# Kernel tuning notes

Measured on AMD Instinct MI355X. Metric: run time of the kernel, lower is better.

The kernel has to match this reference:

```python
import jax, jax.numpy as jnp
import numpy as np

NEG_SLOPE = 0.2  # LeakyReLU slope used by GAT attention
EPS = 1e-16


def segment_softmax(scores, seg, num_segments):
    # numerically-stable softmax over edges grouped by destination node
    m = jax.ops.segment_max(scores, seg, num_segments=num_segments)
    ex = jnp.exp(scores - m[seg])
    s = jax.ops.segment_sum(ex, seg, num_segments=num_segments)
    return ex / (s[seg] + EPS)


def gat_conv(x, edge_index, W, a_src, a_dst, b):
    # x: [N, d_in], edge_index: [2, E], W: [d_in, d_out], a_*: [d_out], b: [d_out]
    n = x.shape[0]
    h = x @ W                                   # [N, d_out]
    src, dst = edge_index[0], edge_index[1]     # [E], [E]
    alpha_src = h @ a_src                       # [N]
    alpha_dst = h @ a_dst                       # [N]
    e = jax.nn.leaky_relu(alpha_src[src] + alpha_dst[dst], NEG_SLOPE)  # [E]
    alpha = segment_softmax(e, dst, n)          # [E]
    out = jax.ops.segment_sum(h[src] * alpha[:, None], dst, num_segments=n)  # [N, d_out]
    return out + b


def setup_inputs() -> dict:
    key = jax.random.key(0)
    ks = jax.random.split(key, 12)
    N, D, E = 100000, 64, 1600000
    x = jax.random.normal(ks[0], (N, D), dtype=jnp.float32)
    edge_index = jax.random.randint(ks[1], (2, E), 0, N, dtype=jnp.int64)
    s = 1.0 / np.sqrt(D)
    W1 = jax.random.normal(ks[2], (D, D), dtype=jnp.float32) * s
    a_src1 = jax.random.normal(ks[3], (D,), dtype=jnp.float32) * s
    a_dst1 = jax.random.normal(ks[4], (D,), dtype=jnp.float32) * s
    b1 = jnp.zeros((D,), dtype=jnp.float32)
    W2 = jax.random.normal(ks[5], (D, D), dtype=jnp.float32) * s
    a_src2 = jax.random.normal(ks[6], (D,), dtype=jnp.float32) * s
    a_dst2 = jax.random.normal(ks[7], (D,), dtype=jnp.float32) * s
    b2 = jnp.zeros((D,), dtype=jnp.float32)
    return {"x": x, "edge_index": edge_index,
            "W1": W1, "a_src1": a_src1, "a_dst1": a_dst1, "b1": b1,
            "W2": W2, "a_src2": a_src2, "a_dst2": a_dst2, "b2": b2}


def reference(x, edge_index, W1, a_src1, a_dst1, b1, W2, a_src2, a_dst2, b2):
    # Encoder.forward: conv_near on first 500 edges, conv_include on the rest
    x = gat_conv(x, edge_index[:, :500], W1, a_src1, a_dst1, b1)
    return gat_conv(x, edge_index[:, 500:], W2, a_src2, a_dst2, b2)
```

## Files before the change

kernel.cpp:

```cpp
#include <hip/hip_runtime.h>


#define LRELU(v) ((v) >= 0.0f ? (v) : 0.2f * (v))
#define EPSF 1e-16f
#define NB 128
#define BCAP 512
#define HSZ 1024

struct P {
    const float* x; const int* EI; int E, N;
    const float *W1, *a_src1, *a_dst1, *b1, *W2, *a_src2, *a_dst2, *b2;
    float* F;
    int* bcnt;
    int* map2;
    float* s_spec;
    float* adsp;
    char* stat;
    int* pkey;
    float* as2tab; float* ad2tab; float* h2tab;
    int* slw; int* nxt;
    float4* out;
    int initBlocks;
};

__device__ __forceinline__ float wred_sum(float v) {
    for (int o = 32; o; o >>= 1) v += __shfl_xor(v, o);
    return v;
}
__device__ __forceinline__ int wred_min(int v) {
    for (int o = 32; o; o >>= 1) v = min(v, __shfl_xor(v, o));
    return v;
}

__global__ __launch_bounds__(256) void k1(P p) {
    const int tid = blockIdx.x * 256 + threadIdx.x;
    const int nth = p.initBlocks * 256;
    for (int i = tid; i < p.N; i += nth) { p.map2[i] = -1; p.s_spec[i] = 0.f; p.stat[i] = 0; }
    for (int i = tid; i < NB * 16; i += nth) p.bcnt[i] = 0;

    const int w = tid >> 6, lane = threadIdx.x & 63;
    if (w >= 500) return;

    float wsl = 0.f, wdl = 0.f, hbl = 0.f;
    for (int l = 0; l < 64; ++l) {
        wsl += p.W1[lane * 64 + l] * p.a_src1[l];
        wdl += p.W1[lane * 64 + l] * p.a_dst1[l];
    }
    for (int k = 0; k < 64; ++k) hbl += p.b1[k] * p.W2[k * 64 + lane];

    if (w == 0) {
        p.F[128 + lane] = hbl;
        float asb = wred_sum(hbl * p.a_src2[lane]);
        float adb = wred_sum(hbl * p.a_dst2[lane]);
        if (lane == 0) { p.F[192] = asb; p.F[193] = adb; }
    }

    const int d = p.EI[p.E + w];
    int firstj = 1 << 30;
    for (int r = 0; r < 8; ++r) {
        int j = r * 64 + lane;
        if (j < 500 && p.EI[p.E + j] == d) firstj = min(firstj, j);
    }
    firstj = wred_min(firstj);
    const bool owner = (firstj == w);
    if (lane == 0) p.pkey[w] = owner ? d : -1;
    if (!owner) return;

    const float dv = wred_sum(p.x[(long)d * 64 + lane] * wdl);
    float Ssum = 0.f, e1w = 0.f, x1l = 0.f;
    bool fm = true;
    for (int r = 0; r < 8; ++r) {
        int j = r * 64 + lane;
        bool m = (j < 500) && (p.EI[p.E + j] == d);
        unsigned long long mask = __ballot(m);
        while (mask) {
            int j0 = r * 64 + (int)__ffsll(mask) - 1;
            mask &= mask - 1;
            int sj = p.EI[j0];
            float xs = p.x[(long)sj * 64 + lane];
            float e1j = LRELU(wred_sum(xs * wsl) + dv);
            float ew;
            if (fm) { e1w = e1j; ew = 1.f; fm = false; }
            else ew = expf(e1j - e1w);
            Ssum += ew;
            float h1l = 0.f;
            #pragma unroll
            for (int k = 0; k < 64; ++k) h1l = fmaf(__shfl(xs, k), p.W1[k * 64 + lane], h1l);
            x1l = fmaf(ew, h1l, x1l);
        }
    }
    float x1 = x1l / (Ssum + EPSF) + p.b1[lane];
    float h2l = 0.f;
    #pragma unroll
    for (int k = 0; k < 64; ++k) h2l = fmaf(__shfl(x1, k), p.W2[k * 64 + lane], h2l);
    p.h2tab[w * 64 + lane] = h2l - hbl;
    float as = wred_sum(h2l * p.a_src2[lane]);
    float ad = wred_sum(h2l * p.a_dst2[lane]);
    if (lane == 0) { p.as2tab[w] = as; p.ad2tab[w] = ad; }
}

__device__ __forceinline__ int hlookup(const int* hkey, const int* hval, int x) {
    unsigned idx = ((unsigned)x * 2654435761u) >> 22;
    while (true) {
        int k = hkey[idx];
        if (k == -1) return -1;
        if (k == x) return hval[idx];
        idx = (idx + 1) & (HSZ - 1);
    }
}

__device__ __forceinline__ void specEdge(const P& p, long e, int s, int bkt,
                                         float asb, float adb,
                                         const int* hkey, const int* hval) {
    int sl = hlookup(hkey, hval, s);
    if (sl < 0) return;
    int d = p.EI[p.E + e];
    int jd = hlookup(hkey, hval, d);
    float ad2v = (jd >= 0) ? p.ad2tab[jd] : adb;
    float md  = LRELU(asb + ad2v);
    float esp = LRELU(p.as2tab[sl] + ad2v);
    atomicAdd(&p.s_spec[d], expf(esp - md) - 1.0f);
    p.stat[d] = 2;
    p.adsp[d] = ad2v;
    int i = atomicAdd(&p.bcnt[bkt * 16], 1);
    if (i < BCAP) {
        int pos = bkt * BCAP + i;
        p.slw[pos] = sl;
        p.nxt[pos] = atomicExch(&p.map2[d], pos);
    }
}

__global__ __launch_bounds__(256) void k2(P p) {
    __shared__ int hkey[HSZ];
    __shared__ int hval[HSZ];
    for (int i = threadIdx.x; i < HSZ; i += 256) hkey[i] = -1;
    __syncthreads();
    for (int i = threadIdx.x; i < 500; i += 256) {
        int key = p.pkey[i];
        if (key >= 0) {
            unsigned idx = ((unsigned)key * 2654435761u) >> 22;
            while (true) {
                int old = atomicCAS(&hkey[idx], -1, key);
                if (old == -1) { hval[idx] = i; break; }
                idx = (idx + 1) & (HSZ - 1);
            }
        }
    }
    __syncthreads();
    const float asb = p.F[192], adb = p.F[193];
    long q = (long)blockIdx.x * 256 + threadIdx.x;
    long base = 500 + q * 4;
    if (base >= p.E) return;
    int bkt = (int)(q & (NB - 1));
    if (base + 3 < p.E) {
        int4 s4 = *(const int4*)(p.EI + base);
        specEdge(p, base + 0, s4.x, bkt, asb, adb, hkey, hval);
        specEdge(p, base + 1, s4.y, bkt, asb, adb, hkey, hval);
        specEdge(p, base + 2, s4.z, bkt, asb, adb, hkey, hval);
        specEdge(p, base + 3, s4.w, bkt, asb, adb, hkey, hval);
    } else {
        for (long e = base; e < p.E; ++e) specEdge(p, e, p.EI[e], bkt, asb, adb, hkey, hval);
    }
}

__device__ __forceinline__ void dstEdge(const P& p, int d) {
    char st = p.stat[d];
    if (st == 0) p.stat[d] = 1;
    else if (st == 2) atomicAdd(&p.s_spec[d], 1.0f);
}

__global__ __launch_bounds__(256) void k3(P p) {
    long q = (long)blockIdx.x * 256 + threadIdx.x;
    long base = 500 + q * 4;
    if (base >= p.E) return;
    if (base + 3 < p.E) {
        int4 d4 = *(const int4*)(p.EI + p.E + base);
        dstEdge(p, d4.x); dstEdge(p, d4.y); dstEdge(p, d4.z); dstEdge(p, d4.w);
    } else {
        for (long e = base; e < p.E; ++e) dstEdge(p, p.EI[p.E + e]);
    }
}

__global__ __launch_bounds__(256) void k4(P p) {
    long t = (long)blockIdx.x * 256 + threadIdx.x;
    if (t >= (long)p.N * 16) return;
    int n = (int)(t >> 4), qq = (int)(t & 15);
    char st = p.stat[n];
    float coef = (st != 0) ? 1.0f : 0.0f;
    float4 hb4 = ((const float4*)(p.F + 128))[qq];
    float4 b24 = ((const float4*)p.b2)[qq];
    float4 o;
    o.x = b24.x + coef * hb4.x; o.y = b24.y + coef * hb4.y;
    o.z = b24.z + coef * hb4.z; o.w = b24.w + coef * hb4.w;
    if (st == 2) {
        float den = p.s_spec[n] + EPSF;
        float ad2v = p.adsp[n];
        float md = LRELU(p.F[192] + ad2v);
        int pos = p.map2[n];
        while (pos >= 0) {
            int sl = p.slw[pos];
            float w = expf(LRELU(p.as2tab[sl] + ad2v) - md) / den;
            float4 h4 = ((const float4*)(p.h2tab + sl * 64))[qq];
            o.x = fmaf(w, h4.x, o.x); o.y = fmaf(w, h4.y, o.y);
            o.z = fmaf(w, h4.z, o.z); o.w = fmaf(w, h4.w, o.w);
            pos = p.nxt[pos];
        }
    }
    p.out[t] = o;
}

extern "C" void kernel_launch(void* const* d_in, const int* in_sizes, int n_in,
                              void* d_out, int out_size, void* d_ws, size_t ws_size,
                              hipStream_t stream) {
    P p;
    p.x      = (const float*)d_in[0];
    p.EI     = (const int*)d_in[1];
    p.W1     = (const float*)d_in[2];
    p.a_src1 = (const float*)d_in[3];
    p.a_dst1 = (const float*)d_in[4];
    p.b1     = (const float*)d_in[5];
    p.W2     = (const float*)d_in[6];
    p.a_src2 = (const float*)d_in[7];
    p.a_dst2 = (const float*)d_in[8];
    p.b2     = (const float*)d_in[9];
    p.out    = (float4*)d_out;
    p.N = in_sizes[0] / 64;
    p.E = in_sizes[1] / 2;

    char* base = (char*)d_ws;
    p.F      = (float*)base;
    p.bcnt   = (int*)(base + 1024);
    p.map2   = p.bcnt + NB * 16;
    p.s_spec = (float*)(p.map2 + p.N);
    p.adsp   = p.s_spec + p.N;
    p.stat   = (char*)(p.adsp + p.N);
    char* q  = p.stat + p.N;
    q = (char*)(((uintptr_t)q + 63) & ~(uintptr_t)63);
    p.pkey   = (int*)q;
    p.as2tab = (float*)(p.pkey + 512);
    p.ad2tab = p.as2tab + 512;
    p.h2tab  = p.ad2tab + 512;
    p.slw    = (int*)(p.h2tab + 512 * 64);
    p.nxt    = p.slw + NB * BCAP;

    p.initBlocks = (p.N + 255) / 256;

    long quads = ((long)p.E - 500 + 3) / 4;
    int scanBlocks = (int)((quads + 255) / 256);

    k1<<<p.initBlocks, 256, 0, stream>>>(p);
    k2<<<scanBlocks, 256, 0, stream>>>(p);
    k3<<<scanBlocks, 256, 0, stream>>>(p);
    k4<<<(int)(((long)p.N * 16 + 255) / 256), 256, 0, stream>>>(p);
}
```

Baseline: 65.13 us.

## Replace per-block shared hash table with dense global node-index map

Each of the ~6000 scan blocks used to rebuild a 1024-entry shared-memory hash table from the 500 layer-1 keys and probe it for every edge. The change writes a dense N-sized idx_map in global memory from the layer-1 kernel, so each edge does a direct indexed load instead of a hash probe. To make that map valid before the scan, the fused init/layer-1 kernel is split into a separate init kernel and a layer-1 kernel, which adds one launch. The idx_map lookups are random global reads (400KB, likely cache-resident) in place of LDS probes.

```diff
diff --git a/kernel.cpp b/kernel.cpp
--- a/kernel.cpp
+++ b/kernel.cpp
@@ -5,22 +5,20 @@
 #define EPSF 1e-16f
 #define NB 128
 #define BCAP 512
-#define HSZ 1024
 
 struct P {
     const float* x; const int* EI; int E, N;
     const float *W1, *a_src1, *a_dst1, *b1, *W2, *a_src2, *a_dst2, *b2;
     float* F;
     int* bcnt;
+    int* idx_map;
     int* map2;
     float* s_spec;
     float* adsp;
     char* stat;
-    int* pkey;
     float* as2tab; float* ad2tab; float* h2tab;
     int* slw; int* nxt;
     float4* out;
-    int initBlocks;
 };
 
 __device__ __forceinline__ float wred_sum(float v) {
@@ -32,13 +30,24 @@
     return v;
 }
 
-__global__ __launch_bounds__(256) void k1(P p) {
-    const int tid = blockIdx.x * 256 + threadIdx.x;
-    const int nth = p.initBlocks * 256;
-    for (int i = tid; i < p.N; i += nth) { p.map2[i] = -1; p.s_spec[i] = 0.f; p.stat[i] = 0; }
-    for (int i = tid; i < NB * 16; i += nth) p.bcnt[i] = 0;
-
-    const int w = tid >> 6, lane = threadIdx.x & 63;
+__global__ __launch_bounds__(256) void initk(P p) {
+    int i = blockIdx.x * 256 + threadIdx.x;
+    if (i < p.N) { p.idx_map[i] = -1; p.map2[i] = -1; p.s_spec[i] = 0.f; p.stat[i] = 0; }
+    if (i < NB * 16) p.bcnt[i] = 0;
+    if (blockIdx.x == 0 && threadIdx.x < 64) {
+        int t = threadIdx.x;
+        float hb = 0.f;
+        for (int k = 0; k < 64; ++k) hb += p.b1[k] * p.W2[k * 64 + t];
+        p.F[128 + t] = hb;
+        float as = wred_sum(hb * p.a_src2[t]);
+        float ad = wred_sum(hb * p.a_dst2[t]);
+        if (t == 0) { p.F[192] = as; p.F[193] = ad; }
+    }
+}
+
+__global__ __launch_bounds__(256) void l1k(P p) {
+    const int w = (blockIdx.x * 256 + threadIdx.x) >> 6;
+    const int lane = threadIdx.x & 63;
     if (w >= 500) return;
 
     float wsl = 0.f, wdl = 0.f, hbl = 0.f;
@@ -47,13 +56,6 @@
         wdl += p.W1[lane * 64 + l] * p.a_dst1[l];
     }
     for (int k = 0; k < 64; ++k) hbl += p.b1[k] * p.W2[k * 64 + lane];
-
-    if (w == 0) {
-        p.F[128 + lane] = hbl;
-        float asb = wred_sum(hbl * p.a_src2[lane]);
-        float adb = wred_sum(hbl * p.a_dst2[lane]);
-        if (lane == 0) { p.F[192] = asb; p.F[193] = adb; }
-    }
 
     const int d = p.EI[p.E + w];
     int firstj = 1 << 30;
@@ -62,9 +64,8 @@
         if (j < 500 && p.EI[p.E + j] == d) firstj = min(firstj, j);
     }
     firstj = wred_min(firstj);
-    const bool owner = (firstj == w);
-    if (lane == 0) p.pkey[w] = owner ? d : -1;
-    if (!owner) return;
+    if (firstj != w) return;
+    if (lane == 0) p.idx_map[d] = w;
 
     const float dv = wred_sum(p.x[(long)d * 64 + lane] * wdl);
     float Ssum = 0.f, e1w = 0.f, x1l = 0.f;
@@ -99,23 +100,12 @@
     if (lane == 0) { p.as2tab[w] = as; p.ad2tab[w] = ad; }
 }
 
-__device__ __forceinline__ int hlookup(const int* hkey, const int* hval, int x) {
-    unsigned idx = ((unsigned)x * 2654435761u) >> 22;
-    while (true) {
-        int k = hkey[idx];
-        if (k == -1) return -1;
-        if (k == x) return hval[idx];
-        idx = (idx + 1) & (HSZ - 1);
-    }
-}
-
 __device__ __forceinline__ void specEdge(const P& p, long e, int s, int bkt,
-                                         float asb, float adb,
-                                         const int* hkey, const int* hval) {
-    int sl = hlookup(hkey, hval, s);
+                                         float asb, float adb) {
+    int sl = p.idx_map[s];
     if (sl < 0) return;
     int d = p.EI[p.E + e];
-    int jd = hlookup(hkey, hval, d);
+    int jd = p.idx_map[d];
     float ad2v = (jd >= 0) ? p.ad2tab[jd] : adb;
     float md  = LRELU(asb + ad2v);
     float esp = LRELU(p.as2tab[sl] + ad2v);
@@ -130,36 +120,20 @@
     }
 }
 
-__global__ __launch_bounds__(256) void k2(P p) {
-    __shared__ int hkey[HSZ];
-    __shared__ int hval[HSZ];
-    for (int i = threadIdx.x; i < HSZ; i += 256) hkey[i] = -1;
-    __syncthreads();
-    for (int i = threadIdx.x; i < 500; i += 256) {
-        int key = p.pkey[i];
-        if (key >= 0) {
-            unsigned idx = ((unsigned)key * 2654435761u) >> 22;
-            while (true) {
-                int old = atomicCAS(&hkey[idx], -1, key);
-                if (old == -1) { hval[idx] = i; break; }
-                idx = (idx + 1) & (HSZ - 1);
-            }
-        }
-    }
-    __syncthreads();
-    const float asb = p.F[192], adb = p.F[193];
+__global__ __launch_bounds__(256) void scanAk(P p) {
     long q = (long)blockIdx.x * 256 + threadIdx.x;
     long base = 500 + q * 4;
     if (base >= p.E) return;
+    const float asb = p.F[192], adb = p.F[193];
     int bkt = (int)(q & (NB - 1));
     if (base + 3 < p.E) {
         int4 s4 = *(const int4*)(p.EI + base);
-        specEdge(p, base + 0, s4.x, bkt, asb, adb, hkey, hval);
-        specEdge(p, base + 1, s4.y, bkt, asb, adb, hkey, hval);
-        specEdge(p, base + 2, s4.z, bkt, asb, adb, hkey, hval);
-        specEdge(p, base + 3, s4.w, bkt, asb, adb, hkey, hval);
+        specEdge(p, base + 0, s4.x, bkt, asb, adb);
+        specEdge(p, base + 1, s4.y, bkt, asb, adb);
+        specEdge(p, base + 2, s4.z, bkt, asb, adb);
+        specEdge(p, base + 3, s4.w, bkt, asb, adb);
     } else {
-        for (long e = base; e < p.E; ++e) specEdge(p, e, p.EI[e], bkt, asb, adb, hkey, hval);
+        for (long e = base; e < p.E; ++e) specEdge(p, e, p.EI[e], bkt, asb, adb);
     }
 }
 
@@ -169,7 +143,7 @@
     else if (st == 2) atomicAdd(&p.s_spec[d], 1.0f);
 }
 
-__global__ __launch_bounds__(256) void k3(P p) {
+__global__ __launch_bounds__(256) void scanBk(P p) {
     long q = (long)blockIdx.x * 256 + threadIdx.x;
     long base = 500 + q * 4;
     if (base >= p.E) return;
@@ -181,7 +155,7 @@
     }
 }
 
-__global__ __launch_bounds__(256) void k4(P p) {
+__global__ __launch_bounds__(256) void outk(P p) {
     long t = (long)blockIdx.x * 256 + threadIdx.x;
     if (t >= (long)p.N * 16) return;
     int n = (int)(t >> 4), qq = (int)(t & 15);
@@ -228,28 +202,27 @@
     p.E = in_sizes[1] / 2;
 
     char* base = (char*)d_ws;
-    p.F      = (float*)base;
-    p.bcnt   = (int*)(base + 1024);
-    p.map2   = p.bcnt + NB * 16;
-    p.s_spec = (float*)(p.map2 + p.N);
-    p.adsp   = p.s_spec + p.N;
-    p.stat   = (char*)(p.adsp + p.N);
-    char* q  = p.stat + p.N;
+    p.F       = (float*)base;
+    p.bcnt    = (int*)(base + 1024);
+    p.idx_map = p.bcnt + NB * 16;
+    p.map2    = p.idx_map + p.N;
+    p.s_spec  = (float*)(p.map2 + p.N);
+    p.adsp    = p.s_spec + p.N;
+    p.stat    = (char*)(p.adsp + p.N);
+    char* q   = p.stat + p.N;
     q = (char*)(((uintptr_t)q + 63) & ~(uintptr_t)63);
-    p.pkey   = (int*)q;
-    p.as2tab = (float*)(p.pkey + 512);
-    p.ad2tab = p.as2tab + 512;
-    p.h2tab  = p.ad2tab + 512;
-    p.slw    = (int*)(p.h2tab + 512 * 64);
-    p.nxt    = p.slw + NB * BCAP;
-
-    p.initBlocks = (p.N + 255) / 256;
+    p.as2tab  = (float*)q;
+    p.ad2tab  = p.as2tab + 512;
+    p.h2tab   = p.ad2tab + 512;
+    p.slw     = (int*)(p.h2tab + 512 * 64);
+    p.nxt     = p.slw + NB * BCAP;
 
     long quads = ((long)p.E - 500 + 3) / 4;
     int scanBlocks = (int)((quads + 255) / 256);
 
-    k1<<<p.initBlocks, 256, 0, stream>>>(p);
-    k2<<<scanBlocks, 256, 0, stream>>>(p);
-    k3<<<scanBlocks, 256, 0, stream>>>(p);
-    k4<<<(int)(((long)p.N * 16 + 255) / 256), 256, 0, stream>>>(p);
-}
+    initk <<<(p.N + 255) / 256, 256, 0, stream>>>(p);
+    l1k   <<<125, 256, 0, stream>>>(p);
+    scanAk<<<scanBlocks, 256, 0, stream>>>(p);
+    scanBk<<<scanBlocks, 256, 0, stream>>>(p);
+    outk  <<<(int)(((long)p.N * 16 + 255) / 256), 256, 0, stream>>>(p);
+}
```

Result: faster. 61.57 us (-5.5%).
